# Kernel tuning notes

Hardware: AMD Instinct MI355X
Metric: run time of the kernel (lower is better)

## Reference

```python
import jax, jax.numpy as jnp
import numpy as np

N_NODES = 100000
N_EDGES = 1600000
D_FEAT = 64


def setup_inputs() -> dict:
    key = jax.random.key(0)
    k1, k2, k3, k4 = jax.random.split(key, 4)
    features = jax.random.normal(k1, (N_NODES, D_FEAT), dtype=jnp.float32)
    edge_weights = jax.random.uniform(k2, (N_EDGES,), dtype=jnp.float32)
    neighbor_idx = jax.random.randint(k3, (N_EDGES,), 0, N_NODES, dtype=jnp.int32)
    segment_ids = jnp.sort(jax.random.randint(k4, (N_EDGES,), 0, N_NODES, dtype=jnp.int32))
    return {"features": features, "edge_weights": edge_weights,
            "neighbor_idx": neighbor_idx, "segment_ids": segment_ids}


def reference(features, edge_weights, neighbor_idx, segment_ids):
    n = features.shape[0]
    # Per-destination-node weight sum and degree.
    wsum = jax.ops.segment_sum(edge_weights, segment_ids, num_segments=n)  # [N]
    deg = jax.ops.segment_sum(jnp.ones_like(edge_weights), segment_ids, num_segments=n)  # [N]
    # If a node's weight sum is 0, fall back to unweighted mean (weight=1, denom=deg).
    use_mean = wsum == 0.0  # [N]
    eff_w = jnp.where(use_mean[segment_ids], 1.0, edge_weights)  # [E]
    gathered = features[neighbor_idx]  # [E, D] gather
    num = jax.ops.segment_sum(eff_w[:, None] * gathered, segment_ids, num_segments=n)  # [N, D]
    den = jnp.where(use_mean, deg, wsum)
    den = jnp.where(den == 0.0, 1.0, den)  # empty nodes -> zeros output
    return num / den[:, None]
```

## Files before the change

kernel.cpp:

```cpp
#include <hip/hip_runtime.h>


#define D_FEAT 64

__global__ __launch_bounds__(256) void WA_build_offsets_kernel(
        const int* __restrict__ seg, int* __restrict__ offs, int N, int E) {
    const int tid = blockIdx.x * blockDim.x + threadIdx.x;
    if (tid > E) return;
    const int cur  = (tid == E) ? N : seg[tid];
    const int prev = (tid == 0) ? -1 : seg[tid - 1];
    for (int v = prev + 1; v <= cur; ++v) offs[v] = tid;
}

__global__ __launch_bounds__(256) void WeightedAggregator_28424093564968_kernel(
        const float* __restrict__ feat,
        const float* __restrict__ ew,
        const int*   __restrict__ nidx,
        const int*   __restrict__ offs,
        float*       __restrict__ out,
        int N) {
    const int gwave = (blockIdx.x * blockDim.x + threadIdx.x) >> 6;
    const int lane  = threadIdx.x & 63;
    const int slot  = lane >> 4;
    const int dofs  = (lane & 15) << 2;

    const int  n  = gwave * 4 + slot;
    const bool vn = n < N;

    const int start = vn ? offs[n]     : 0;
    const int end   = vn ? offs[n + 1] : 0;
    const int deg   = end - start;

    float ws = 0.0f;
    float awx = 0.f, awy = 0.f, awz = 0.f, aww = 0.f;
    float aux = 0.f, auy = 0.f, auz = 0.f, auw = 0.f;

    for (int k = 0; __any(k < deg); k += 4) {
        #pragma unroll
        for (int j = 0; j < 4; ++j) {
            const int  kk = k + j;
            const bool v  = kk < deg;
            const int  e  = v ? (start + kk) : 0;
            const int  id = v ? nidx[e] : 0;
            const float w = v ? ew[e]   : 0.0f;
            const float s = v ? 1.0f    : 0.0f;
            const float4 f = *(const float4*)(feat + (size_t)id * D_FEAT + dofs);
            ws  += w;
            awx += w * f.x; awy += w * f.y; awz += w * f.z; aww += w * f.w;
            aux += s * f.x; auy += s * f.y; auz += s * f.z; auw += s * f.w;
        }
    }

    const bool use_mean = (ws == 0.0f);
    float den = use_mean ? (float)deg : ws;
    if (den == 0.0f) den = 1.0f;
    const float inv = 1.0f / den;

    if (vn) {
        float4 r;
        r.x = (use_mean ? aux : awx) * inv;
        r.y = (use_mean ? auy : awy) * inv;
        r.z = (use_mean ? auz : awz) * inv;
        r.w = (use_mean ? auw : aww) * inv;
        *(float4*)(out + (size_t)n * D_FEAT + dofs) = r;
    }
}

__global__ __launch_bounds__(256) void WA_search_kernel(
        const float* __restrict__ feat, const float* __restrict__ ew,
        const int* __restrict__ nidx, const int* __restrict__ seg,
        float* __restrict__ out, int N, int E) {
    const int wave = (blockIdx.x * blockDim.x + threadIdx.x) >> 6;
    const int lane = threadIdx.x & 63;
    if (wave >= N) return;
    const int n = wave;

    int lo = 0, hi = E;
    while (hi - lo > 64) {
        const long long span = hi - lo;
        const int p = lo + (int)((span * (lane + 1)) / 65);
        const bool ge = seg[p] >= n;
        const unsigned long long mask = __ballot(ge);
        if (mask == 0ull) {
            lo = lo + (int)((span * 64) / 65);
        } else {
            const int first = __ffsll((long long)mask) - 1;
            const int nhi = lo + (int)((span * (first + 1)) / 65);
            const int nlo = (first == 0) ? lo : lo + (int)((span * first) / 65);
            lo = nlo; hi = nhi;
        }
    }
    {
        const int p = lo + lane;
        const bool ge = (p >= hi) || (seg[p] >= n);
        const unsigned long long mask = __ballot(ge);
        lo = (mask == 0ull) ? hi : lo + __ffsll((long long)mask) - 1;
    }
    const int start = lo;
    int end = start;
    for (;;) {
        const int p = end + lane;
        const bool stop = (p >= E) || (seg[p] > n);
        const unsigned long long mask = __ballot(stop);
        if (mask) { end += __ffsll((long long)mask) - 1; break; }
        end += 64;
    }

    float ws = 0.0f;
    for (int e = start + lane; e < end; e += 64) ws += ew[e];
    #pragma unroll
    for (int off = 32; off > 0; off >>= 1) ws += __shfl_xor(ws, off);
    const bool use_mean = (ws == 0.0f);
    float den = use_mean ? (float)(end - start) : ws;
    if (den == 0.0f) den = 1.0f;

    const int slot = lane >> 4;
    const int dofs = (lane & 15) << 2;
    float ax = 0.f, ay = 0.f, az = 0.f, aw = 0.f;
    for (int e = start; e < end; e += 8) {
        const int p0 = e + slot, p1 = e + 4 + slot;
        const bool v0 = p0 < end, v1 = p1 < end;
        const int  i0 = v0 ? nidx[p0] : 0;
        const int  i1 = v1 ? nidx[p1] : 0;
        const float w0 = v0 ? (use_mean ? 1.0f : ew[p0]) : 0.0f;
        const float w1 = v1 ? (use_mean ? 1.0f : ew[p1]) : 0.0f;
        const float4 f0 = *(const float4*)(feat + (size_t)i0 * D_FEAT + dofs);
        const float4 f1 = *(const float4*)(feat + (size_t)i1 * D_FEAT + dofs);
        ax += w0 * f0.x; ay += w0 * f0.y; az += w0 * f0.z; aw += w0 * f0.w;
        ax += w1 * f1.x; ay += w1 * f1.y; az += w1 * f1.z; aw += w1 * f1.w;
    }
    #pragma unroll
    for (int m = 16; m <= 32; m <<= 1) {
        ax += __shfl_xor(ax, m); ay += __shfl_xor(ay, m);
        az += __shfl_xor(az, m); aw += __shfl_xor(aw, m);
    }
    if (slot == 0) {
        const float inv = 1.0f / den;
        float4 r; r.x = ax*inv; r.y = ay*inv; r.z = az*inv; r.w = aw*inv;
        *(float4*)(out + (size_t)n * D_FEAT + dofs) = r;
    }
}

extern "C" void kernel_launch(void* const* d_in, const int* in_sizes, int n_in,
                              void* d_out, int out_size, void* d_ws, size_t ws_size,
                              hipStream_t stream) {
    const float* feat = (const float*)d_in[0];
    const float* ew   = (const float*)d_in[1];
    const int*   nidx = (const int*)d_in[2];
    const int*   seg  = (const int*)d_in[3];
    float*       out  = (float*)d_out;

    const int E = in_sizes[1];
    const int N = in_sizes[0] / D_FEAT;

    if (ws_size >= (size_t)(N + 1) * sizeof(int)) {
        int* offs = (int*)d_ws;
        const int g1 = (E + 1 + 255) / 256;
        WA_build_offsets_kernel<<<g1, 256, 0, stream>>>(seg, offs, N, E);
        const int nodes_per_block = 16;
        const int grid = (N + nodes_per_block - 1) / nodes_per_block;
        WeightedAggregator_28424093564968_kernel<<<grid, 256, 0, stream>>>(
            feat, ew, nidx, offs, out, N);
    } else {
        const int grid = (N + 3) / 4;
        WA_search_kernel<<<grid, 256, 0, stream>>>(feat, ew, nidx, seg, out, N, E);
    }
}
```

Baseline: 147.1 us.

## Map one wave per node with scalar per-lane feature loads

Replaces the four-nodes-per-wave layout (16 lanes per node, float4 loads) with one wave per node, where each lane handles one feature column and edges are walked serially with an unroll of eight. Edge index and weight loads become wave-uniform, so they can be scalar loads, and the divergent __any loop over the largest degree in the wave goes away. In exchange each gather is a 4-byte-per-lane load instead of float4, and fewer edges are in flight per wave. The search fallback gets the same per-lane simplification.

```diff
diff --git a/kernel.cpp b/kernel.cpp
--- a/kernel.cpp
+++ b/kernel.cpp
@@ -19,51 +19,44 @@
         const int*   __restrict__ offs,
         float*       __restrict__ out,
         int N) {
-    const int gwave = (blockIdx.x * blockDim.x + threadIdx.x) >> 6;
-    const int lane  = threadIdx.x & 63;
-    const int slot  = lane >> 4;
-    const int dofs  = (lane & 15) << 2;
+    const int wave = (blockIdx.x * blockDim.x + threadIdx.x) >> 6;
+    const int lane = threadIdx.x & 63;
+    if (wave >= N) return;
 
-    const int  n  = gwave * 4 + slot;
-    const bool vn = n < N;
-
-    const int start = vn ? offs[n]     : 0;
-    const int end   = vn ? offs[n + 1] : 0;
+    const int start = offs[wave];
+    const int end   = offs[wave + 1];
     const int deg   = end - start;
 
     float ws = 0.0f;
-    float awx = 0.f, awy = 0.f, awz = 0.f, aww = 0.f;
-    float aux = 0.f, auy = 0.f, auz = 0.f, auw = 0.f;
+    float aw = 0.0f;
+    float au = 0.0f;
 
-    for (int k = 0; __any(k < deg); k += 4) {
+    int e = start;
+    for (; e + 8 <= end; e += 8) {
         #pragma unroll
-        for (int j = 0; j < 4; ++j) {
-            const int  kk = k + j;
-            const bool v  = kk < deg;
-            const int  e  = v ? (start + kk) : 0;
-            const int  id = v ? nidx[e] : 0;
-            const float w = v ? ew[e]   : 0.0f;
-            const float s = v ? 1.0f    : 0.0f;
-            const float4 f = *(const float4*)(feat + (size_t)id * D_FEAT + dofs);
-            ws  += w;
-            awx += w * f.x; awy += w * f.y; awz += w * f.z; aww += w * f.w;
-            aux += s * f.x; auy += s * f.y; auz += s * f.z; auw += s * f.w;
+        for (int j = 0; j < 8; ++j) {
+            const int   id = nidx[e + j];
+            const float w  = ew[e + j];
+            const float f  = feat[(size_t)id * D_FEAT + lane];
+            ws += w;
+            aw += w * f;
+            au += f;
         }
+    }
+    for (; e < end; ++e) {
+        const int   id = nidx[e];
+        const float w  = ew[e];
+        const float f  = feat[(size_t)id * D_FEAT + lane];
+        ws += w;
+        aw += w * f;
+        au += f;
     }
 
     const bool use_mean = (ws == 0.0f);
     float den = use_mean ? (float)deg : ws;
     if (den == 0.0f) den = 1.0f;
-    const float inv = 1.0f / den;
 
-    if (vn) {
-        float4 r;
-        r.x = (use_mean ? aux : awx) * inv;
-        r.y = (use_mean ? auy : awy) * inv;
-        r.z = (use_mean ? auz : awz) * inv;
-        r.w = (use_mean ? auw : aww) * inv;
-        *(float4*)(out + (size_t)n * D_FEAT + dofs) = r;
-    }
+    out[(size_t)wave * D_FEAT + lane] = (use_mean ? au : aw) / den;
 }
 
 __global__ __launch_bounds__(256) void WA_search_kernel(
@@ -114,31 +107,13 @@
     float den = use_mean ? (float)(end - start) : ws;
     if (den == 0.0f) den = 1.0f;
 
-    const int slot = lane >> 4;
-    const int dofs = (lane & 15) << 2;
-    float ax = 0.f, ay = 0.f, az = 0.f, aw = 0.f;
-    for (int e = start; e < end; e += 8) {
-        const int p0 = e + slot, p1 = e + 4 + slot;
-        const bool v0 = p0 < end, v1 = p1 < end;
-        const int  i0 = v0 ? nidx[p0] : 0;
-        const int  i1 = v1 ? nidx[p1] : 0;
-        const float w0 = v0 ? (use_mean ? 1.0f : ew[p0]) : 0.0f;
-        const float w1 = v1 ? (use_mean ? 1.0f : ew[p1]) : 0.0f;
-        const float4 f0 = *(const float4*)(feat + (size_t)i0 * D_FEAT + dofs);
-        const float4 f1 = *(const float4*)(feat + (size_t)i1 * D_FEAT + dofs);
-        ax += w0 * f0.x; ay += w0 * f0.y; az += w0 * f0.z; aw += w0 * f0.w;
-        ax += w1 * f1.x; ay += w1 * f1.y; az += w1 * f1.z; aw += w1 * f1.w;
+    float aw = 0.0f;
+    for (int e = start; e < end; ++e) {
+        const int   id = nidx[e];
+        const float w  = use_mean ? 1.0f : ew[e];
+        aw += w * feat[(size_t)id * D_FEAT + lane];
     }
-    #pragma unroll
-    for (int m = 16; m <= 32; m <<= 1) {
-        ax += __shfl_xor(ax, m); ay += __shfl_xor(ay, m);
-        az += __shfl_xor(az, m); aw += __shfl_xor(aw, m);
-    }
-    if (slot == 0) {
-        const float inv = 1.0f / den;
-        float4 r; r.x = ax*inv; r.y = ay*inv; r.z = az*inv; r.w = aw*inv;
-        *(float4*)(out + (size_t)n * D_FEAT + dofs) = r;
-    }
+    out[(size_t)n * D_FEAT + lane] = aw / den;
 }
 
 extern "C" void kernel_launch(void* const* d_in, const int* in_sizes, int n_in,
@@ -153,16 +128,15 @@
     const int E = in_sizes[1];
     const int N = in_sizes[0] / D_FEAT;
 
+    const int grid = (N + 3) / 4;
+
     if (ws_size >= (size_t)(N + 1) * sizeof(int)) {
         int* offs = (int*)d_ws;
         const int g1 = (E + 1 + 255) / 256;
         WA_build_offsets_kernel<<<g1, 256, 0, stream>>>(seg, offs, N, E);
-        const int nodes_per_block = 16;
-        const int grid = (N + nodes_per_block - 1) / nodes_per_block;
         WeightedAggregator_28424093564968_kernel<<<grid, 256, 0, stream>>>(
             feat, ew, nidx, offs, out, N);
     } else {
-        const int grid = (N + 3) / 4;
         WA_search_kernel<<<grid, 256, 0, stream>>>(feat, ew, nidx, seg, out, N, E);
     }
 }
```

After: 156.6 us. 1.07x slower.
